# Kernel tuning notes

Hardware: AMD Instinct MI355X
Metric: run time of the kernel (lower is better)

The kernel has to match this reference:

```python
import jax, jax.numpy as jnp
import numpy as np

C = 1024
D = C // 8      # query/key channels
R = C // 16     # channel-attention reduction
B, H, W = 4, 64, 64


def setup_inputs() -> dict:
    key = jax.random.key(0)
    ks = jax.random.split(key, 10)
    s = lambda k, shp, fan: jax.random.normal(k, shp, jnp.float32) * (1.0 / np.sqrt(fan))
    return {
        "x": jax.random.normal(ks[0], (B, C, H, W), jnp.float32),
        "x1": jax.random.normal(ks[1], (B, C, H, W), jnp.float32),
        "Wq": s(ks[2], (D, C), C), "bq": jnp.zeros((D,), jnp.float32),
        "Wk": s(ks[3], (D, C), C), "bk": jnp.zeros((D,), jnp.float32),
        "Wv": s(ks[4], (C, C), C), "bv": jnp.zeros((C,), jnp.float32),
        "Wca1": s(ks[5], (R, C), C),  # CBAM MLP, no bias
        "Wca2": s(ks[6], (C, R), R),
    }


def _forward(x, x1, Wq, bq, Wk, bk, Wv, bv, Wca1, Wca2):
    b, c, h, w = x.shape
    n = h * w
    # 1x1 convs as channel matmuls
    Q = (jnp.einsum('bchw,dc->bdhw', x, Wq) + bq[:, None, None]).reshape(b, D, n)   # [B,D,N]
    K = (jnp.einsum('bchw,dc->bdhw', x, Wk) + bk[:, None, None]).reshape(b, D, n)   # [B,D,N]
    V = (jnp.einsum('bchw,oc->bohw', x1, Wv) + bv[:, None, None]).reshape(b, c, n)  # [B,C,N]
    # energy[b,n,m] = Q[:,n] . K[:,m]
    energy = jnp.einsum('bdn,bdm->bnm', Q, K)
    att = jax.nn.sigmoid(energy)                       # [B,N,N]
    # torch: bmm(V, att^T) -> out[b,c,n] = sum_m V[b,c,m] * att[b,n,m]
    out = jnp.einsum('bcm,bnm->bcn', V, att).reshape(b, c, h, w)
    # ChannelAttention (CBAM): shared MLP on avg+max pooled features, sigmoid gate
    avg = out.mean(axis=(2, 3))                        # [B,C]
    mx = out.max(axis=(2, 3))                          # [B,C]
    mlp = lambda v: jnp.einsum('cr,br->bc', Wca2, jax.nn.relu(jnp.einsum('rc,bc->br', Wca1, v)))
    gate = jax.nn.sigmoid(mlp(avg) + mlp(mx))          # [B,C]
    return out * gate[:, :, None, None]


def reference(x, x1, Wq, bq, Wk, bk, Wv, bv, Wca1, Wca2):
    return _forward(x, x1, Wq, bq, Wk, bk, Wv, bv, Wca1, Wca2)
```

## Files before the change

### kernel.cpp

```cpp
#include <hip/hip_runtime.h>
#include <hip/hip_fp16.h>
#include <cstdint>

typedef _Float16 f16;
typedef __attribute__((ext_vector_type(8))) _Float16 half8;
typedef __attribute__((ext_vector_type(4))) float floatx4;

#define CC 1024
#define DD 128
#define RRR 64
#define BBATCH 4
#define NNN 4096

#define BM 128
#define BN 128
#define BK 64

__device__ __forceinline__ void gl_lds16(const void* g, void* l) {
  __builtin_amdgcn_global_load_lds(
      (__attribute__((address_space(1))) void*)(uintptr_t)g,
      (__attribute__((address_space(3))) void*)l, 16, 0, 0);
}

template<int EPI>
__global__ __launch_bounds__(256)
void gemm_bt(const f16* __restrict__ A, const f16* __restrict__ Bp, void* __restrict__ Cout,
             const float* __restrict__ bias, int M, int N, int K,
             int lda, int ldb, int ldc, size_t sA, size_t sB, size_t sC)
{
  __shared__ __align__(16) f16 As[BM * BK];
  __shared__ __align__(16) f16 Bs[BN * BK];
  const int z = blockIdx.z;
  A  += (size_t)z * sA;
  Bp += (size_t)z * sB;

  const int tid  = threadIdx.x;
  const int lane = tid & 63;
  const int wave = tid >> 6;
  const int m0 = blockIdx.y * BM;
  const int n0 = blockIdx.x * BN;
  const int wm = (wave >> 1) * 64;
  const int wn = (wave & 1) * 64;

  floatx4 acc[4][4];
#pragma unroll
  for (int i = 0; i < 4; ++i)
#pragma unroll
    for (int j = 0; j < 4; ++j)
      acc[i][j] = (floatx4){0.f, 0.f, 0.f, 0.f};

  const int srow = lane >> 3;
  const int sgr  = ((lane & 7) ^ srow) * 8;
  const int sdst = (lane & 7) * 8;
  const f16* aB = A  + (size_t)m0 * lda;
  const f16* bB = Bp + (size_t)n0 * ldb;

  const int quad = lane >> 4;
  const int r16  = lane & 15;
  const int rs   = r16 & 7;

  for (int k0 = 0; k0 < K; k0 += BK) {
#pragma unroll
    for (int r = 0; r < 4; ++r) {
      const int row = (r * 4 + wave) * 8 + srow;
      gl_lds16(aB + (size_t)row * lda + k0 + sgr, As + row * BK + sdst);
      gl_lds16(bB + (size_t)row * ldb + k0 + sgr, Bs + row * BK + sdst);
    }
    __syncthreads();

#pragma unroll
    for (int kk = 0; kk < BK; kk += 32) {
      const int kg = kk >> 3;
      half8 af[4], bfr[4];
#pragma unroll
      for (int i = 0; i < 4; ++i)
        af[i] = *(const half8*)(As + (wm + i * 16 + r16) * BK + (((quad + kg) ^ rs) * 8));
#pragma unroll
      for (int j = 0; j < 4; ++j)
        bfr[j] = *(const half8*)(Bs + (wn + j * 16 + r16) * BK + (((quad + kg) ^ rs) * 8));
#pragma unroll
      for (int i = 0; i < 4; ++i)
#pragma unroll
        for (int j = 0; j < 4; ++j)
          acc[i][j] = __builtin_amdgcn_mfma_f32_16x16x32_f16(af[i], bfr[j], acc[i][j], 0, 0, 0);
    }
    __syncthreads();
  }

  float* Cf = (EPI == 0) ? ((float*)Cout + (size_t)z * sC) : nullptr;
  f16*   Ch = (EPI != 0) ? ((f16*)Cout   + (size_t)z * sC) : nullptr;
#pragma unroll
  for (int i = 0; i < 4; ++i) {
#pragma unroll
    for (int r = 0; r < 4; ++r) {
      const int row = m0 + wm + i * 16 + quad * 4 + r;
#pragma unroll
      for (int j = 0; j < 4; ++j) {
        const int col = n0 + wn + j * 16 + r16;
        float v = acc[i][j][r];
        if constexpr (EPI == 0) {
          Cf[(size_t)row * ldc + col] = v;
        } else if constexpr (EPI == 1) {
          Ch[(size_t)row * ldc + col] = (f16)(v + bias[row]);
        } else if constexpr (EPI == 2) {
          Ch[(size_t)row * ldc + col] = (f16)(v + bias[col]);
        } else {
          Ch[(size_t)row * ldc + col] = (f16)(1.0f / (1.0f + __expf(-v)));
        }
      }
    }
  }
}

__global__ __launch_bounds__(256)
void transpose_cvt(const float* __restrict__ in, f16* __restrict__ out, int rows, int cols)
{
  const size_t zo = (size_t)blockIdx.z * rows * cols;
  in += zo; out += zo;
  __shared__ float tile[32][33];
  const int c0 = blockIdx.y * 32;
  const int n0 = blockIdx.x * 32;
  const int tx = threadIdx.x & 31;
  const int ty = threadIdx.x >> 5;
#pragma unroll
  for (int r = 0; r < 32; r += 8)
    tile[ty + r][tx] = in[(size_t)(c0 + ty + r) * cols + n0 + tx];
  __syncthreads();
#pragma unroll
  for (int r = 0; r < 32; r += 8)
    out[(size_t)(n0 + ty + r) * rows + c0 + tx] = (f16)tile[tx][ty + r];
}

__global__ __launch_bounds__(256)
void cvt_f16(const float* __restrict__ in, f16* __restrict__ out, int n)
{
  int i = blockIdx.x * 256 + threadIdx.x;
  if (i < n) out[i] = (f16)in[i];
}

__global__ void concat_bias(const float* __restrict__ a, const float* __restrict__ b,
                            float* __restrict__ o)
{
  int t = threadIdx.x;
  o[t] = (t < 128) ? a[t] : b[t - 128];
}

__global__ __launch_bounds__(256)
void rowreduce(const float* __restrict__ X, float* __restrict__ avg, float* __restrict__ mx, int ncols)
{
  const size_t ridx = (size_t)blockIdx.y * gridDim.x + blockIdx.x;
  const float4* p = (const float4*)(X + ridx * ncols);
  float s = 0.f, m = -3.402823466e38f;
  for (int i = threadIdx.x; i < ncols / 4; i += 256) {
    float4 v = p[i];
    s += v.x + v.y + v.z + v.w;
    m = fmaxf(m, fmaxf(fmaxf(v.x, v.y), fmaxf(v.z, v.w)));
  }
#pragma unroll
  for (int o = 32; o > 0; o >>= 1) {
    s += __shfl_down(s, o);
    m = fmaxf(m, __shfl_down(m, o));
  }
  __shared__ float ss[4], sm[4];
  if ((threadIdx.x & 63) == 0) { ss[threadIdx.x >> 6] = s; sm[threadIdx.x >> 6] = m; }
  __syncthreads();
  if (threadIdx.x == 0) {
    s = ss[0] + ss[1] + ss[2] + ss[3];
    m = fmaxf(fmaxf(sm[0], sm[1]), fmaxf(sm[2], sm[3]));
    avg[ridx] = s / (float)ncols;
    mx[ridx] = m;
  }
}

__global__ __launch_bounds__(256)
void mlp_gate(const float* __restrict__ avg, const float* __restrict__ mxv,
              const float* __restrict__ W1 , const float* __restrict__ W2 ,
              float* __restrict__ gate)
{
  const int z = blockIdx.x;
  avg += (size_t)z * CC; mxv += (size_t)z * CC; gate += (size_t)z * CC;
  const int t = threadIdx.x;
  const int r = t & 63;
  const int part = t >> 6;
  __shared__ float pa[4][64], pm[4][64], h[RRR];
  {
    const float* w = W1 + (size_t)r * CC + part * 256;
    const float* av = avg + part * 256;
    const float* mv = mxv + part * 256;
    float sa = 0.f, sm = 0.f;
    for (int c = 0; c < 256; ++c) { float wv = w[c]; sa += wv * av[c]; sm += wv * mv[c]; }
    pa[part][r] = sa; pm[part][r] = sm;
  }
  __syncthreads();
  if (t < RRR) {
    float A_ = pa[0][t] + pa[1][t] + pa[2][t] + pa[3][t];
    float M_ = pm[0][t] + pm[1][t] + pm[2][t] + pm[3][t];
    h[t] = fmaxf(A_, 0.f) + fmaxf(M_, 0.f);
  }
  __syncthreads();
  for (int c = t; c < CC; c += 256) {
    float s = 0.f;
    for (int rr = 0; rr < RRR; ++rr) s += W2[(size_t)c * RRR + rr] * h[rr];
    gate[c] = 1.0f / (1.0f + __expf(-s));
  }
}

__global__ __launch_bounds__(256)
void scale_out(float* __restrict__ out, const float* __restrict__ gate)
{
  out  += (size_t)blockIdx.y * CC * NNN;
  gate += (size_t)blockIdx.y * CC;
  size_t i = (size_t)blockIdx.x * 256 + threadIdx.x;
  float4* p = (float4*)out;
  const float g = gate[(i * 4) >> 12];
  float4 v = p[i];
  v.x *= g; v.y *= g; v.z *= g; v.w *= g;
  p[i] = v;
}

extern "C" void kernel_launch(void* const* d_in, const int* in_sizes, int n_in,
                              void* d_out, int out_size, void* d_ws, size_t ws_size,
                              hipStream_t stream)
{
  const float* x    = (const float*)d_in[0];
  const float* x1   = (const float*)d_in[1];
  const float* Wq   = (const float*)d_in[2];
  const float* bq   = (const float*)d_in[3];
  const float* Wk   = (const float*)d_in[4];
  const float* bk   = (const float*)d_in[5];
  const float* Wv   = (const float*)d_in[6];
  const float* bv   = (const float*)d_in[7];
  const float* Wca1 = (const float*)d_in[8];
  const float* Wca2 = (const float*)d_in[9];
  float* out = (float*)d_out;

  char* ws = (char*)d_ws;
  size_t off = 0;
  auto alloc = [&](size_t bytes) { void* p = ws + off; off += (bytes + 255) & ~255ULL; return p; };

  f16* WQKb = (f16*)alloc((size_t)2 * DD * CC * 2);
  f16* Wvb  = (f16*)alloc((size_t)CC * CC * 2);
  float* bqk  = (float*)alloc(256 * 4);
  float* avg  = (float*)alloc((size_t)BBATCH * CC * 4);
  float* mxv  = (float*)alloc((size_t)BBATCH * CC * 4);
  float* gate = (float*)alloc((size_t)BBATCH * CC * 4);

  const size_t attB  = (size_t)NNN * NNN * 2;
  const size_t xTB   = (size_t)BBATCH * NNN * CC * 2;
  const size_t qkB   = (size_t)BBATCH * NNN * 2 * DD * 2;
  const size_t vBB   = (size_t)BBATCH * CC * NNN * 2;
  const size_t fixedEnd = off;

  int g = 0;
  for (int cand = BBATCH; cand >= 1; cand >>= 1) {
    size_t need = fixedEnd + 2 * xTB + qkB + vBB + (size_t)cand * attB + (1 << 20);
    if (need <= ws_size) { g = cand; break; }
  }

  const dim3 blk(256);
  cvt_f16<<<(DD * CC + 255) / 256, blk, 0, stream>>>(Wq, WQKb, DD * CC);
  cvt_f16<<<(DD * CC + 255) / 256, blk, 0, stream>>>(Wk, WQKb + (size_t)DD * CC, DD * CC);
  cvt_f16<<<(CC * CC + 255) / 256, blk, 0, stream>>>(Wv, Wvb, CC * CC);
  concat_bias<<<1, blk, 0, stream>>>(bq, bk, bqk);

  if (g > 0) {
    f16* xTb  = (f16*)alloc(xTB);
    f16* x1Tb = (f16*)alloc(xTB);
    f16* QKt  = (f16*)alloc(qkB);
    f16* Vb   = (f16*)alloc(vBB);
    f16* att  = (f16*)alloc((size_t)g * attB);

    transpose_cvt<<<dim3(NNN / 32, CC / 32, BBATCH), blk, 0, stream>>>(x,  xTb,  CC, NNN);
    transpose_cvt<<<dim3(NNN / 32, CC / 32, BBATCH), blk, 0, stream>>>(x1, x1Tb, CC, NNN);

    gemm_bt<2><<<dim3(2 * DD / BN, NNN / BM, BBATCH), blk, 0, stream>>>(
        xTb, WQKb, QKt, bqk, NNN, 2 * DD, CC,
        CC, CC, 2 * DD, (size_t)NNN * CC, 0, (size_t)NNN * 2 * DD);
    gemm_bt<1><<<dim3(NNN / BN, CC / BM, BBATCH), blk, 0, stream>>>(
        Wvb, x1Tb, Vb, bv, CC, NNN, CC,
        CC, CC, NNN, 0, (size_t)NNN * CC, (size_t)CC * NNN);

    for (int b0 = 0; b0 < BBATCH; b0 += g) {
      const int gc = (b0 + g <= BBATCH) ? g : (BBATCH - b0);
      const size_t sQK = (size_t)NNN * 2 * DD;
      gemm_bt<3><<<dim3(NNN / BN, NNN / BM, gc), blk, 0, stream>>>(
          QKt + (size_t)b0 * sQK, QKt + (size_t)b0 * sQK + DD, att, nullptr,
          NNN, NNN, DD, 2 * DD, 2 * DD, NNN, sQK, sQK, (size_t)NNN * NNN);
      gemm_bt<0><<<dim3(NNN / BN, CC / BM, gc), blk, 0, stream>>>(
          Vb + (size_t)b0 * CC * NNN, att, out + (size_t)b0 * CC * NNN, nullptr,
          CC, NNN, NNN, NNN, NNN, NNN,
          (size_t)CC * NNN, (size_t)NNN * NNN, (size_t)CC * NNN);
    }

    rowreduce<<<dim3(CC, BBATCH), blk, 0, stream>>>(out, avg, mxv, NNN);
    mlp_gate<<<BBATCH, blk, 0, stream>>>(avg, mxv, Wca1, Wca2, gate);
    scale_out<<<dim3(CC * NNN / 4 / 256, BBATCH), blk, 0, stream>>>(out, gate);
  } else {
    f16* xTb  = (f16*)alloc((size_t)NNN * CC * 2);
    f16* x1Tb = (f16*)alloc((size_t)NNN * CC * 2);
    f16* QKt  = (f16*)alloc((size_t)NNN * 2 * DD * 2);
    f16* Vb   = (f16*)alloc((size_t)CC * NNN * 2);
    f16* att  = (f16*)alloc(attB);

    for (int b = 0; b < BBATCH; ++b) {
      const float* xb  = x  + (size_t)b * CC * NNN;
      const float* x1b = x1 + (size_t)b * CC * NNN;
      float* outb = out + (size_t)b * CC * NNN;

      transpose_cvt<<<dim3(NNN / 32, CC / 32, 1), blk, 0, stream>>>(xb,  xTb,  CC, NNN);
      transpose_cvt<<<dim3(NNN / 32, CC / 32, 1), blk, 0, stream>>>(x1b, x1Tb, CC, NNN);

      gemm_bt<2><<<dim3(2 * DD / BN, NNN / BM, 1), blk, 0, stream>>>(
          xTb, WQKb, QKt, bqk, NNN, 2 * DD, CC, CC, CC, 2 * DD, 0, 0, 0);
      gemm_bt<1><<<dim3(NNN / BN, CC / BM, 1), blk, 0, stream>>>(
          Wvb, x1Tb, Vb, bv, CC, NNN, CC, CC, CC, NNN, 0, 0, 0);
      gemm_bt<3><<<dim3(NNN / BN, NNN / BM, 1), blk, 0, stream>>>(
          QKt, QKt + DD, att, nullptr, NNN, NNN, DD, 2 * DD, 2 * DD, NNN, 0, 0, 0);
      gemm_bt<0><<<dim3(NNN / BN, CC / BM, 1), blk, 0, stream>>>(
          Vb, att, outb, nullptr, CC, NNN, NNN, NNN, NNN, NNN, 0, 0, 0);

      rowreduce<<<dim3(CC, 1), blk, 0, stream>>>(outb, avg + (size_t)b * CC, mxv + (size_t)b * CC, NNN);
      mlp_gate<<<1, blk, 0, stream>>>(avg + (size_t)b * CC, mxv + (size_t)b * CC, Wca1, Wca2, gate + (size_t)b * CC);
      scale_out<<<dim3(CC * NNN / 4 / 256, 1), blk, 0, stream>>>(outb, gate + (size_t)b * CC);
    }
  }
}
```

Baseline: 563.7 us.

## Stage f16 GEMM epilogue through LDS, use BK=128 for QK, merge prep kernels

```diff
diff --git a/kernel.cpp b/kernel.cpp
--- a/kernel.cpp
+++ b/kernel.cpp
@@ -14,7 +14,6 @@
 
 #define BM 128
 #define BN 128
-#define BK 64
 
 __device__ __forceinline__ void gl_lds16(const void* g, void* l) {
   __builtin_amdgcn_global_load_lds(
@@ -22,18 +21,20 @@
       (__attribute__((address_space(3))) void*)l, 16, 0, 0);
 }
 
-template<int EPI>
+template<int EPI, int BKT>
 __global__ __launch_bounds__(256)
 void gemm_bt(const f16* __restrict__ A, const f16* __restrict__ Bp, void* __restrict__ Cout,
              const float* __restrict__ bias, int M, int N, int K,
              int lda, int ldb, int ldc, size_t sA, size_t sB, size_t sC)
 {
-  __shared__ __align__(16) f16 As[BM * BK];
-  __shared__ __align__(16) f16 Bs[BN * BK];
+  constexpr int GPR = BKT / 8;
+  constexpr int LOG2GPR = (BKT == 64) ? 3 : 4;
+  constexpr int GIT = (BM * GPR) / 256;
+  __shared__ __align__(16) f16 S[2 * BM * BKT];
+  f16* As = S;
+  f16* Bs = S + BM * BKT;
+
   const int z = blockIdx.z;
-  A  += (size_t)z * sA;
-  Bp += (size_t)z * sB;
-
   const int tid  = threadIdx.x;
   const int lane = tid & 63;
   const int wave = tid >> 6;
@@ -41,43 +42,48 @@
   const int n0 = blockIdx.x * BN;
   const int wm = (wave >> 1) * 64;
   const int wn = (wave & 1) * 64;
-
-  floatx4 acc[4][4];
-#pragma unroll
-  for (int i = 0; i < 4; ++i)
-#pragma unroll
-    for (int j = 0; j < 4; ++j)
-      acc[i][j] = (floatx4){0.f, 0.f, 0.f, 0.f};
-
-  const int srow = lane >> 3;
-  const int sgr  = ((lane & 7) ^ srow) * 8;
-  const int sdst = (lane & 7) * 8;
-  const f16* aB = A  + (size_t)m0 * lda;
-  const f16* bB = Bp + (size_t)n0 * ldb;
-
   const int quad = lane >> 4;
   const int r16  = lane & 15;
   const int rs   = r16 & 7;
 
-  for (int k0 = 0; k0 < K; k0 += BK) {
-#pragma unroll
-    for (int r = 0; r < 4; ++r) {
-      const int row = (r * 4 + wave) * 8 + srow;
-      gl_lds16(aB + (size_t)row * lda + k0 + sgr, As + row * BK + sdst);
-      gl_lds16(bB + (size_t)row * ldb + k0 + sgr, Bs + row * BK + sdst);
+  const f16* Ab = A  + (size_t)z * sA + (size_t)m0 * lda;
+  const f16* Bb = Bp + (size_t)z * sB + (size_t)n0 * ldb;
+
+  floatx4 acc[4][4];
+#pragma unroll
+  for (int i = 0; i < 4; ++i)
+#pragma unroll
+    for (int j = 0; j < 4; ++j)
+      acc[i][j] = (floatx4){0.f, 0.f, 0.f, 0.f};
+
+  int srow[GIT], ssrc[GIT];
+#pragma unroll
+  for (int r = 0; r < GIT; ++r) {
+    const int gi = r * 256 + tid;
+    const int row = gi >> LOG2GPR;
+    const int gc  = gi & (GPR - 1);
+    srow[r] = row;
+    ssrc[r] = ((gc ^ (row & 7)) << 3);
+  }
+
+  for (int k0 = 0; k0 < K; k0 += BKT) {
+#pragma unroll
+    for (int r = 0; r < GIT; ++r) {
+      gl_lds16(Ab + (size_t)srow[r] * lda + k0 + ssrc[r], As + (size_t)(r * 256 + tid) * 8);
+      gl_lds16(Bb + (size_t)srow[r] * ldb + k0 + ssrc[r], Bs + (size_t)(r * 256 + tid) * 8);
     }
     __syncthreads();
 
 #pragma unroll
-    for (int kk = 0; kk < BK; kk += 32) {
+    for (int kk = 0; kk < BKT; kk += 32) {
       const int kg = kk >> 3;
       half8 af[4], bfr[4];
 #pragma unroll
       for (int i = 0; i < 4; ++i)
-        af[i] = *(const half8*)(As + (wm + i * 16 + r16) * BK + (((quad + kg) ^ rs) * 8));
+        af[i] = *(const half8*)(As + (wm + i * 16 + r16) * BKT + (((quad + kg) ^ rs) << 3));
 #pragma unroll
       for (int j = 0; j < 4; ++j)
-        bfr[j] = *(const half8*)(Bs + (wn + j * 16 + r16) * BK + (((quad + kg) ^ rs) * 8));
+        bfr[j] = *(const half8*)(Bs + (wn + j * 16 + r16) * BKT + (((quad + kg) ^ rs) << 3));
 #pragma unroll
       for (int i = 0; i < 4; ++i)
 #pragma unroll
@@ -87,36 +93,73 @@
     __syncthreads();
   }
 
-  float* Cf = (EPI == 0) ? ((float*)Cout + (size_t)z * sC) : nullptr;
-  f16*   Ch = (EPI != 0) ? ((f16*)Cout   + (size_t)z * sC) : nullptr;
-#pragma unroll
-  for (int i = 0; i < 4; ++i) {
-#pragma unroll
-    for (int r = 0; r < 4; ++r) {
-      const int row = m0 + wm + i * 16 + quad * 4 + r;
-#pragma unroll
-      for (int j = 0; j < 4; ++j) {
-        const int col = n0 + wn + j * 16 + r16;
-        float v = acc[i][j][r];
-        if constexpr (EPI == 0) {
-          Cf[(size_t)row * ldc + col] = v;
-        } else if constexpr (EPI == 1) {
-          Ch[(size_t)row * ldc + col] = (f16)(v + bias[row]);
-        } else if constexpr (EPI == 2) {
-          Ch[(size_t)row * ldc + col] = (f16)(v + bias[col]);
-        } else {
-          Ch[(size_t)row * ldc + col] = (f16)(1.0f / (1.0f + __expf(-v)));
+  if constexpr (EPI == 0) {
+    float* Cf = (float*)Cout + (size_t)z * sC;
+#pragma unroll
+    for (int i = 0; i < 4; ++i)
+#pragma unroll
+      for (int r = 0; r < 4; ++r) {
+        const int row = m0 + wm + i * 16 + quad * 4 + r;
+#pragma unroll
+        for (int j = 0; j < 4; ++j)
+          Cf[(size_t)row * ldc + n0 + wn + j * 16 + r16] = acc[i][j][r];
+      }
+  } else {
+    f16* Ch = (f16*)Cout + (size_t)z * sC;
+    f16* Ct = S;
+#pragma unroll
+    for (int i = 0; i < 4; ++i)
+#pragma unroll
+      for (int r = 0; r < 4; ++r) {
+        const int rl = wm + i * 16 + quad * 4 + r;
+#pragma unroll
+        for (int j = 0; j < 4; ++j) {
+          const int cl = wn + j * 16 + r16;
+          const float v = acc[i][j][r];
+          f16 h;
+          if constexpr (EPI == 1)      h = (f16)(v + bias[m0 + rl]);
+          else if constexpr (EPI == 2) h = (f16)(v + bias[n0 + cl]);
+          else                         h = (f16)(1.0f / (1.0f + __expf(-v)));
+          Ct[rl * BN + ((((cl >> 3) ^ (rl & 7)) << 3) | (cl & 7))] = h;
         }
       }
-    }
-  }
-}
-
-__global__ __launch_bounds__(256)
-void transpose_cvt(const float* __restrict__ in, f16* __restrict__ out, int rows, int cols)
-{
-  const size_t zo = (size_t)blockIdx.z * rows * cols;
-  in += zo; out += zo;
+    __syncthreads();
+#pragma unroll
+    for (int p = 0; p < 8; ++p) {
+      const int idx = p * 256 + tid;
+      const int rl = idx >> 4;
+      const int g  = idx & 15;
+      half8 vv = *(const half8*)(Ct + rl * BN + (((g ^ (rl & 7))) << 3));
+      *(half8*)(Ch + (size_t)(m0 + rl) * ldc + n0 + g * 8) = vv;
+    }
+  }
+}
+
+__global__ __launch_bounds__(256)
+void prep(const float* __restrict__ Wq, const float* __restrict__ Wk, const float* __restrict__ Wv,
+          const float* __restrict__ bq, const float* __restrict__ bk,
+          f16* __restrict__ WQKb, f16* __restrict__ Wvb, float* __restrict__ bqk)
+{
+  const int NV = CC * CC;
+  const int NQ = DD * CC;
+  int i = blockIdx.x * 256 + threadIdx.x;
+  if (i < NV)                    Wvb[i] = (f16)Wv[i];
+  else if (i < NV + NQ)          WQKb[i - NV] = (f16)Wq[i - NV];
+  else if (i < NV + 2 * NQ)      WQKb[i - NV] = (f16)Wk[i - NV - NQ];
+  else if (i < NV + 2 * NQ + 2 * DD) {
+    int t = i - NV - 2 * NQ;
+    bqk[t] = (t < DD) ? bq[t] : bk[t - DD];
+  }
+}
+
+__global__ __launch_bounds__(256)
+void transpose_cvt(const float* __restrict__ x, const float* __restrict__ x1,
+                   f16* __restrict__ ox, f16* __restrict__ ox1, int nb)
+{
+  const int zz = blockIdx.z;
+  const int b  = (zz < nb) ? zz : zz - nb;
+  const float* in = ((zz < nb) ? x : x1) + (size_t)b * CC * NNN;
+  f16* out = ((zz < nb) ? ox : ox1) + (size_t)b * CC * NNN;
   __shared__ float tile[32][33];
   const int c0 = blockIdx.y * 32;
   const int n0 = blockIdx.x * 32;
@@ -124,25 +167,11 @@
   const int ty = threadIdx.x >> 5;
 #pragma unroll
   for (int r = 0; r < 32; r += 8)
-    tile[ty + r][tx] = in[(size_t)(c0 + ty + r) * cols + n0 + tx];
+    tile[ty + r][tx] = in[(size_t)(c0 + ty + r) * NNN + n0 + tx];
   __syncthreads();
 #pragma unroll
   for (int r = 0; r < 32; r += 8)
-    out[(size_t)(n0 + ty + r) * rows + c0 + tx] = (f16)tile[tx][ty + r];
-}
-
-__global__ __launch_bounds__(256)
-void cvt_f16(const float* __restrict__ in, f16* __restrict__ out, int n)
-{
-  int i = blockIdx.x * 256 + threadIdx.x;
-  if (i < n) out[i] = (f16)in[i];
-}
-
-__global__ void concat_bias(const float* __restrict__ a, const float* __restrict__ b,
-                            float* __restrict__ o)
-{
-  int t = threadIdx.x;
-  o[t] = (t < 128) ? a[t] : b[t - 128];
+    out[(size_t)(n0 + ty + r) * CC + c0 + tx] = (f16)tile[tx][ty + r];
 }
 
 __global__ __launch_bounds__(256)
@@ -174,7 +203,7 @@
 
 __global__ __launch_bounds__(256)
 void mlp_gate(const float* __restrict__ avg, const float* __restrict__ mxv,
-              const float* __restrict__ W1 , const float* __restrict__ W2 ,
+              const float* __restrict__ W1, const float* __restrict__ W2,
               float* __restrict__ gate)
 {
   const int z = blockIdx.x;
@@ -245,10 +274,10 @@
   float* mxv  = (float*)alloc((size_t)BBATCH * CC * 4);
   float* gate = (float*)alloc((size_t)BBATCH * CC * 4);
 
-  const size_t attB  = (size_t)NNN * NNN * 2;
-  const size_t xTB   = (size_t)BBATCH * NNN * CC * 2;
-  const size_t qkB   = (size_t)BBATCH * NNN * 2 * DD * 2;
-  const size_t vBB   = (size_t)BBATCH * CC * NNN * 2;
+  const size_t attB = (size_t)NNN * NNN * 2;
+  const size_t xTB  = (size_t)BBATCH * NNN * CC * 2;
+  const size_t qkB  = (size_t)BBATCH * NNN * 2 * DD * 2;
+  const size_t vBB  = (size_t)BBATCH * CC * NNN * 2;
   const size_t fixedEnd = off;
 
   int g = 0;
@@ -258,10 +287,8 @@
   }
 
   const dim3 blk(256);
-  cvt_f16<<<(DD * CC + 255) / 256, blk, 0, stream>>>(Wq, WQKb, DD * CC);
-  cvt_f16<<<(DD * CC + 255) / 256, blk, 0, stream>>>(Wk, WQKb + (size_t)DD * CC, DD * CC);
-  cvt_f16<<<(CC * CC + 255) / 256, blk, 0, stream>>>(Wv, Wvb, CC * CC);
-  concat_bias<<<1, blk, 0, stream>>>(bq, bk, bqk);
+  const int prepN = CC * CC + 2 * DD * CC + 2 * DD;
+  prep<<<(prepN + 255) / 256, blk, 0, stream>>>(Wq, Wk, Wv, bq, bk, WQKb, Wvb, bqk);
 
   if (g > 0) {
     f16* xTb  = (f16*)alloc(xTB);
@@ -270,23 +297,22 @@
     f16* Vb   = (f16*)alloc(vBB);
     f16* att  = (f16*)alloc((size_t)g * attB);
 
-    transpose_cvt<<<dim3(NNN / 32, CC / 32, BBATCH), blk, 0, stream>>>(x,  xTb,  CC, NNN);
-    transpose_cvt<<<dim3(NNN / 32, CC / 32, BBATCH), blk, 0, stream>>>(x1, x1Tb, CC, NNN);
-
-    gemm_bt<2><<<dim3(2 * DD / BN, NNN / BM, BBATCH), blk, 0, stream>>>(
+    transpose_cvt<<<dim3(NNN / 32, CC / 32, 2 * BBATCH), blk, 0, stream>>>(x, x1, xTb, x1Tb, BBATCH);
+
+    gemm_bt<2, 64><<<dim3(2 * DD / BN, NNN / BM, BBATCH), blk, 0, stream>>>(
         xTb, WQKb, QKt, bqk, NNN, 2 * DD, CC,
         CC, CC, 2 * DD, (size_t)NNN * CC, 0, (size_t)NNN * 2 * DD);
-    gemm_bt<1><<<dim3(NNN / BN, CC / BM, BBATCH), blk, 0, stream>>>(
+    gemm_bt<1, 64><<<dim3(NNN / BN, CC / BM, BBATCH), blk, 0, stream>>>(
         Wvb, x1Tb, Vb, bv, CC, NNN, CC,
         CC, CC, NNN, 0, (size_t)NNN * CC, (size_t)CC * NNN);
 
     for (int b0 = 0; b0 < BBATCH; b0 += g) {
       const int gc = (b0 + g <= BBATCH) ? g : (BBATCH - b0);
       const size_t sQK = (size_t)NNN * 2 * DD;
-      gemm_bt<3><<<dim3(NNN / BN, NNN / BM, gc), blk, 0, stream>>>(
+      gemm_bt<3, 128><<<dim3(NNN / BN, NNN / BM, gc), blk, 0, stream>>>(
           QKt + (size_t)b0 * sQK, QKt + (size_t)b0 * sQK + DD, att, nullptr,
           NNN, NNN, DD, 2 * DD, 2 * DD, NNN, sQK, sQK, (size_t)NNN * NNN);
-      gemm_bt<0><<<dim3(NNN / BN, CC / BM, gc), blk, 0, stream>>>(
+      gemm_bt<0, 64><<<dim3(NNN / BN, CC / BM, gc), blk, 0, stream>>>(
           Vb + (size_t)b0 * CC * NNN, att, out + (size_t)b0 * CC * NNN, nullptr,
           CC, NNN, NNN, NNN, NNN, NNN,
           (size_t)CC * NNN, (size_t)NNN * NNN, (size_t)CC * NNN);
@@ -307,16 +333,15 @@
       const float* x1b = x1 + (size_t)b * CC * NNN;
       float* outb = out + (size_t)b * CC * NNN;
 
-      transpose_cvt<<<dim3(NNN / 32, CC / 32, 1), blk, 0, stream>>>(xb,  xTb,  CC, NNN);
-      transpose_cvt<<<dim3(NNN / 32, CC / 32, 1), blk, 0, stream>>>(x1b, x1Tb, CC, NNN);
-
-      gemm_bt<2><<<dim3(2 * DD / BN, NNN / BM, 1), blk, 0, stream>>>(
+      transpose_cvt<<<dim3(NNN / 32, CC / 32, 2), blk, 0, stream>>>(xb, x1b, xTb, x1Tb, 1);
+
+      gemm_bt<2, 64><<<dim3(2 * DD / BN, NNN / BM, 1), blk, 0, stream>>>(
           xTb, WQKb, QKt, bqk, NNN, 2 * DD, CC, CC, CC, 2 * DD, 0, 0, 0);
-      gemm_bt<1><<<dim3(NNN / BN, CC / BM, 1), blk, 0, stream>>>(
+      gemm_bt<1, 64><<<dim3(NNN / BN, CC / BM, 1), blk, 0, stream>>>(
           Wvb, x1Tb, Vb, bv, CC, NNN, CC, CC, CC, NNN, 0, 0, 0);
-      gemm_bt<3><<<dim3(NNN / BN, NNN / BM, 1), blk, 0, stream>>>(
+      gemm_bt<3, 128><<<dim3(NNN / BN, NNN / BM, 1), blk, 0, stream>>>(
           QKt, QKt + DD, att, nullptr, NNN, NNN, DD, 2 * DD, 2 * DD, NNN, 0, 0, 0);
-      gemm_bt<0><<<dim3(NNN / BN, CC / BM, 1), blk, 0, stream>>>(
+      gemm_bt<0, 64><<<dim3(NNN / BN, CC / BM, 1), blk, 0, stream>>>(
           Vb, att, outb, nullptr, CC, NNN, NNN, NNN, NNN, NNN, 0, 0, 0);
 
       rowreduce<<<dim3(CC, 1), blk, 0, stream>>>(outb, avg + (size_t)b * CC, mxv + (size_t)b * CC, NNN);
```

Measured after the change: 543.6 us. 3.6% less time.
